# Kernel optimization log

Measured on AMD Instinct MI355X. Metric: run time of the kernel, lower is better.

The kernel has to match this reference:

```python
import jax, jax.numpy as jnp
import numpy as np

N_RAYS = 131072
N_SAMPLES = 128
FEAT_DIM = 3
FAR_DELTA = 1e10  # sentinel delta appended for the last sample, as in the torch code


def setup_inputs() -> dict:
    key = jax.random.key(0)
    k1, k2, k3 = jax.random.split(key, 3)
    # densities are non-negative (output of e.g. relu/softplus in NeRF)
    density = jax.random.uniform(k1, (N_RAYS, N_SAMPLES), dtype=jnp.float32) * 2.0
    feature = jax.random.uniform(k2, (N_RAYS, N_SAMPLES, FEAT_DIM), dtype=jnp.float32)
    # monotonically increasing per-ray sample depths: near + cumsum(uniform bins)
    bins = jax.random.uniform(k3, (N_RAYS, N_SAMPLES), dtype=jnp.float32) * 0.05 + 0.01
    depth_values = 1.0 + jnp.cumsum(bins, axis=1)
    return {"density": density, "feature": feature, "depth_values": depth_values}


def reference(density, feature, depth_values):
    # deltas: consecutive depth differences, with a huge last delta (torch.cat(..., 1e10*ones))
    deltas = jnp.concatenate(
        [depth_values[:, 1:] - depth_values[:, :-1],
         jnp.full_like(depth_values[:, :1], FAR_DELTA)],
        axis=-1,
    )  # [N, S]
    att = jnp.exp(-density * deltas)              # exp(-sigma_i * delta_i), [N, S]
    # inclusive prefix product, matching the loop: T[i] = T[i-1]*exp(-sigma_i*delta_i)
    T = jnp.cumprod(att, axis=1)                  # [N, S]
    weights = T * (1.0 - att)                     # [N, S]
    feat_out = jnp.einsum("ns,nsc->nc", weights, feature)      # [N, 3]
    depth_out = jnp.sum(weights * depth_values, axis=1)         # [N]
    return feat_out, depth_out
```

## Files before the change

### kernel.cpp

```cpp
#include <hip/hip_runtime.h>

#define N_RAYS    131072
#define N_SAMPLES 128
#define FAR_DELTA 1e10f

#define ROW_SHL(n) (0x100 + (n))
#define ROW_SHR(n) (0x110 + (n))
#define QPERM(a,b,c,d) ((a) | ((b) << 2) | ((c) << 4) | ((d) << 6))

template <int CTRL>
__device__ __forceinline__ float dpp_f(float v, float ident) {
    return __int_as_float(__builtin_amdgcn_update_dpp(
        __float_as_int(ident), __float_as_int(v), CTRL, 0xF, 0xF, false));
}

__global__ __launch_bounds__(256) void VolumeRenderer_57612691308835_kernel(
    const float* __restrict__ density,
    const float* __restrict__ feature,
    const float* __restrict__ depth,
    float* __restrict__ out_feat,
    float* __restrict__ out_depth)
{
    const int tid  = threadIdx.x;
    const int wave = tid >> 6;
    const int lane = tid & 63;
    const int p    = lane & 15;
    const int g    = lane >> 4;
    const int ray  = (blockIdx.x << 4) + (wave << 2) + g;

    const long base = (long)ray * N_SAMPLES + p * 8;

    const float4 dn0 = *(const float4*)(density + base);
    const float4 dn1 = *(const float4*)(density + base + 4);
    const float4 dp0 = *(const float4*)(depth + base);
    const float4 dp1 = *(const float4*)(depth + base + 4);
    const float4* fp = (const float4*)(feature + base * 3);
    const float4 f0 = fp[0], f1 = fp[1], f2 = fp[2];
    const float4 f3 = fp[3], f4 = fp[4], f5 = fp[5];

    const float dnext = dpp_f<ROW_SHL(1)>(dp0.x, 0.0f);
    const float d7 = (p == 15) ? FAR_DELTA : (dnext - dp1.w);

    const float a0 = __expf(-dn0.x * (dp0.y - dp0.x));
    const float a1 = __expf(-dn0.y * (dp0.z - dp0.y));
    const float a2 = __expf(-dn0.z * (dp0.w - dp0.z));
    const float a3 = __expf(-dn0.w * (dp1.x - dp0.w));
    const float a4 = __expf(-dn1.x * (dp1.y - dp1.x));
    const float a5 = __expf(-dn1.y * (dp1.z - dp1.y));
    const float a6 = __expf(-dn1.z * (dp1.w - dp1.z));
    const float a7 = __expf(-dn1.w * d7);

    float s = ((a0 * a1) * (a2 * a3)) * ((a4 * a5) * (a6 * a7));
    s *= dpp_f<ROW_SHR(1)>(s, 1.0f);
    s *= dpp_f<ROW_SHR(2)>(s, 1.0f);
    s *= dpp_f<ROW_SHR(4)>(s, 1.0f);
    s *= dpp_f<ROW_SHR(8)>(s, 1.0f);
    float T = dpp_f<ROW_SHR(1)>(s, 1.0f);

    T *= a0; const float w0 = T * (1.0f - a0);
    T *= a1; const float w1 = T * (1.0f - a1);
    T *= a2; const float w2 = T * (1.0f - a2);
    T *= a3; const float w3 = T * (1.0f - a3);
    T *= a4; const float w4 = T * (1.0f - a4);
    T *= a5; const float w5 = T * (1.0f - a5);
    T *= a6; const float w6 = T * (1.0f - a6);
    T *= a7; const float w7 = T * (1.0f - a7);

    float fx = w0*f0.x + w1*f0.w + w2*f1.z + w3*f2.y + w4*f3.x + w5*f3.w + w6*f4.z + w7*f5.y;
    float fy = w0*f0.y + w1*f1.x + w2*f1.w + w3*f2.z + w4*f3.y + w5*f4.x + w6*f4.w + w7*f5.z;
    float fz = w0*f0.z + w1*f1.y + w2*f2.x + w3*f2.w + w4*f3.z + w5*f4.y + w6*f5.x + w7*f5.w;
    float dd = w0*dp0.x + w1*dp0.y + w2*dp0.z + w3*dp0.w + w4*dp1.x + w5*dp1.y + w6*dp1.z + w7*dp1.w;

    fx += dpp_f<ROW_SHL(8)>(fx, 0.0f);
    fy += dpp_f<ROW_SHL(8)>(fy, 0.0f);
    fz += dpp_f<ROW_SHL(8)>(fz, 0.0f);
    dd += dpp_f<ROW_SHL(8)>(dd, 0.0f);
    fx += dpp_f<ROW_SHL(4)>(fx, 0.0f);
    fy += dpp_f<ROW_SHL(4)>(fy, 0.0f);
    fz += dpp_f<ROW_SHL(4)>(fz, 0.0f);
    dd += dpp_f<ROW_SHL(4)>(dd, 0.0f);

    const bool o1 = (p & 1);
    const float sA = o1 ? fx : fy;
    const float rA = dpp_f<QPERM(1, 0, 3, 2)>(sA, 0.0f);
    if (o1) fy += rA; else fx += rA;
    const float sB = o1 ? fz : dd;
    const float rB = dpp_f<QPERM(1, 0, 3, 2)>(sB, 0.0f);
    if (o1) dd += rB; else fz += rB;
    const float own = (p & 2) ? (o1 ? dd : fz) : (o1 ? fy : fx);
    const float sC  = (p & 2) ? (o1 ? fy : fx) : (o1 ? dd : fz);
    const float rC  = dpp_f<QPERM(2, 3, 0, 1)>(sC, 0.0f);
    const float res = own + rC;

    if (p < 3)       out_feat[(long)ray * 3 + p] = res;
    else if (p == 3) out_depth[ray] = res;
}

extern "C" void kernel_launch(void* const* d_in, const int* in_sizes, int n_in,
                              void* d_out, int out_size, void* d_ws, size_t ws_size,
                              hipStream_t stream) {
    const float* density = (const float*)d_in[0];
    const float* feature = (const float*)d_in[1];
    const float* depth   = (const float*)d_in[2];

    float* out_feat  = (float*)d_out;
    float* out_depth = (float*)d_out + (long)N_RAYS * 3;

    const int rays_per_block = 16;
    const int grid = N_RAYS / rays_per_block;
    VolumeRenderer_57612691308835_kernel<<<grid, 256, 0, stream>>>(
        density, feature, depth, out_feat, out_depth);
}
```

Baseline: 352.1 us.

## Persistent waves with register double-buffered coalesced loads staged through LDS

```diff
diff --git a/kernel.cpp b/kernel.cpp
--- a/kernel.cpp
+++ b/kernel.cpp
@@ -3,6 +3,9 @@
 #define N_RAYS    131072
 #define N_SAMPLES 128
 #define FAR_DELTA 1e10f
+
+#define NBLOCKS   1024
+#define ITERS     8
 
 #define ROW_SHL(n) (0x100 + (n))
 #define ROW_SHR(n) (0x110 + (n))
@@ -14,86 +17,162 @@
         __float_as_int(ident), __float_as_int(v), CTRL, 0xF, 0xF, false));
 }
 
-__global__ __launch_bounds__(256) void VolumeRenderer_57612691308835_kernel(
+#define WAVE_LDS  13312
+#define FEAT_STR  112
+#define DD_STR    48
+#define DEN_OFF   7168
+#define DEP_OFF   10240
+
+__global__ __launch_bounds__(256, 3) void VolumeRenderer_57612691308835_kernel(
     const float* __restrict__ density,
     const float* __restrict__ feature,
     const float* __restrict__ depth,
     float* __restrict__ out_feat,
     float* __restrict__ out_depth)
 {
+    __shared__ char lds[4 * WAVE_LDS];
+
     const int tid  = threadIdx.x;
     const int wave = tid >> 6;
     const int lane = tid & 63;
     const int p    = lane & 15;
     const int g    = lane >> 4;
-    const int ray  = (blockIdx.x << 4) + (wave << 2) + g;
 
-    const long base = (long)ray * N_SAMPLES + p * 8;
+    char* wlds = lds + wave * WAVE_LDS;
 
-    const float4 dn0 = *(const float4*)(density + base);
-    const float4 dn1 = *(const float4*)(density + base + 4);
-    const float4 dp0 = *(const float4*)(depth + base);
-    const float4 dp1 = *(const float4*)(depth + base + 4);
-    const float4* fp = (const float4*)(feature + base * 3);
-    const float4 f0 = fp[0], f1 = fp[1], f2 = fp[2];
-    const float4 f3 = fp[3], f4 = fp[4], f5 = fp[5];
+    char* fR  = wlds + lane * FEAT_STR;
+    char* dnR = wlds + DEN_OFF + lane * DD_STR;
+    char* dpR = wlds + DEP_OFF + lane * DD_STR;
 
-    const float dnext = dpp_f<ROW_SHL(1)>(dp0.x, 0.0f);
-    const float d7 = (p == 15) ? FAR_DELTA : (dnext - dp1.w);
+    int wf[6], wdn[2], wdp[2];
+    #pragma unroll
+    for (int c = 0; c < 6; ++c) {
+        const int q  = c * 64 + lane;
+        const int gg = q / 96;
+        const int r  = q - gg * 96;
+        const int pp = r / 6;
+        const int cc = r - pp * 6;
+        wf[c] = gg * (16 * FEAT_STR) + pp * FEAT_STR + cc * 16;
+    }
+    #pragma unroll
+    for (int c = 0; c < 2; ++c) {
+        const int q  = c * 64 + lane;
+        const int gg = q >> 5;
+        const int r  = q & 31;
+        const int pp = r >> 1;
+        const int cc = r & 1;
+        wdn[c] = DEN_OFF + gg * (16 * DD_STR) + pp * DD_STR + cc * 16;
+        wdp[c] = DEP_OFF + gg * (16 * DD_STR) + pp * DD_STR + cc * 16;
+    }
 
-    const float a0 = __expf(-dn0.x * (dp0.y - dp0.x));
-    const float a1 = __expf(-dn0.y * (dp0.z - dp0.y));
-    const float a2 = __expf(-dn0.z * (dp0.w - dp0.z));
-    const float a3 = __expf(-dn0.w * (dp1.x - dp0.w));
-    const float a4 = __expf(-dn1.x * (dp1.y - dp1.x));
-    const float a5 = __expf(-dn1.y * (dp1.z - dp1.y));
-    const float a6 = __expf(-dn1.z * (dp1.w - dp1.z));
-    const float a7 = __expf(-dn1.w * d7);
+    const long wray = ((long)blockIdx.x * 4 + wave) * 32;
+    const float4* fG  = (const float4*)feature + wray * 96 + lane;
+    const float4* dnG = (const float4*)density + wray * 32 + lane;
+    const float4* dpG = (const float4*)depth   + wray * 32 + lane;
 
-    float s = ((a0 * a1) * (a2 * a3)) * ((a4 * a5) * (a6 * a7));
-    s *= dpp_f<ROW_SHR(1)>(s, 1.0f);
-    s *= dpp_f<ROW_SHR(2)>(s, 1.0f);
-    s *= dpp_f<ROW_SHR(4)>(s, 1.0f);
-    s *= dpp_f<ROW_SHR(8)>(s, 1.0f);
-    float T = dpp_f<ROW_SHR(1)>(s, 1.0f);
+    struct Buf { float4 f[6]; float4 dn[2]; float4 dp[2]; };
+    Buf A, B;
 
-    T *= a0; const float w0 = T * (1.0f - a0);
-    T *= a1; const float w1 = T * (1.0f - a1);
-    T *= a2; const float w2 = T * (1.0f - a2);
-    T *= a3; const float w3 = T * (1.0f - a3);
-    T *= a4; const float w4 = T * (1.0f - a4);
-    T *= a5; const float w5 = T * (1.0f - a5);
-    T *= a6; const float w6 = T * (1.0f - a6);
-    T *= a7; const float w7 = T * (1.0f - a7);
+    auto LOAD = [&](Buf& b, int it) {
+        const int fo = it * 384, do_ = it * 128;
+        #pragma unroll
+        for (int c = 0; c < 6; ++c) b.f[c] = fG[fo + c * 64];
+        #pragma unroll
+        for (int c = 0; c < 2; ++c) {
+            b.dn[c] = dnG[do_ + c * 64];
+            b.dp[c] = dpG[do_ + c * 64];
+        }
+    };
 
-    float fx = w0*f0.x + w1*f0.w + w2*f1.z + w3*f2.y + w4*f3.x + w5*f3.w + w6*f4.z + w7*f5.y;
-    float fy = w0*f0.y + w1*f1.x + w2*f1.w + w3*f2.z + w4*f3.y + w5*f4.x + w6*f4.w + w7*f5.z;
-    float fz = w0*f0.z + w1*f1.y + w2*f2.x + w3*f2.w + w4*f3.z + w5*f4.y + w6*f5.x + w7*f5.w;
-    float dd = w0*dp0.x + w1*dp0.y + w2*dp0.z + w3*dp0.w + w4*dp1.x + w5*dp1.y + w6*dp1.z + w7*dp1.w;
+    auto PROC = [&](const Buf& b, int it) {
+        #pragma unroll
+        for (int c = 0; c < 6; ++c) *(float4*)(wlds + wf[c]) = b.f[c];
+        #pragma unroll
+        for (int c = 0; c < 2; ++c) {
+            *(float4*)(wlds + wdn[c]) = b.dn[c];
+            *(float4*)(wlds + wdp[c]) = b.dp[c];
+        }
 
-    fx += dpp_f<ROW_SHL(8)>(fx, 0.0f);
-    fy += dpp_f<ROW_SHL(8)>(fy, 0.0f);
-    fz += dpp_f<ROW_SHL(8)>(fz, 0.0f);
-    dd += dpp_f<ROW_SHL(8)>(dd, 0.0f);
-    fx += dpp_f<ROW_SHL(4)>(fx, 0.0f);
-    fy += dpp_f<ROW_SHL(4)>(fy, 0.0f);
-    fz += dpp_f<ROW_SHL(4)>(fz, 0.0f);
-    dd += dpp_f<ROW_SHL(4)>(dd, 0.0f);
+        const float4 dn0 = *(const float4*)(dnR);
+        const float4 dn1 = *(const float4*)(dnR + 16);
+        const float4 dp0 = *(const float4*)(dpR);
+        const float4 dp1 = *(const float4*)(dpR + 16);
+        const float4 f0 = *(const float4*)(fR);
+        const float4 f1 = *(const float4*)(fR + 16);
+        const float4 f2 = *(const float4*)(fR + 32);
+        const float4 f3 = *(const float4*)(fR + 48);
+        const float4 f4 = *(const float4*)(fR + 64);
+        const float4 f5 = *(const float4*)(fR + 80);
 
-    const bool o1 = (p & 1);
-    const float sA = o1 ? fx : fy;
-    const float rA = dpp_f<QPERM(1, 0, 3, 2)>(sA, 0.0f);
-    if (o1) fy += rA; else fx += rA;
-    const float sB = o1 ? fz : dd;
-    const float rB = dpp_f<QPERM(1, 0, 3, 2)>(sB, 0.0f);
-    if (o1) dd += rB; else fz += rB;
-    const float own = (p & 2) ? (o1 ? dd : fz) : (o1 ? fy : fx);
-    const float sC  = (p & 2) ? (o1 ? fy : fx) : (o1 ? dd : fz);
-    const float rC  = dpp_f<QPERM(2, 3, 0, 1)>(sC, 0.0f);
-    const float res = own + rC;
+        const float dnext = dpp_f<ROW_SHL(1)>(dp0.x, 0.0f);
+        const float d7 = (p == 15) ? FAR_DELTA : (dnext - dp1.w);
 
-    if (p < 3)       out_feat[(long)ray * 3 + p] = res;
-    else if (p == 3) out_depth[ray] = res;
+        const float a0 = __expf(-dn0.x * (dp0.y - dp0.x));
+        const float a1 = __expf(-dn0.y * (dp0.z - dp0.y));
+        const float a2 = __expf(-dn0.z * (dp0.w - dp0.z));
+        const float a3 = __expf(-dn0.w * (dp1.x - dp0.w));
+        const float a4 = __expf(-dn1.x * (dp1.y - dp1.x));
+        const float a5 = __expf(-dn1.y * (dp1.z - dp1.y));
+        const float a6 = __expf(-dn1.z * (dp1.w - dp1.z));
+        const float a7 = __expf(-dn1.w * d7);
+
+        float s = ((a0 * a1) * (a2 * a3)) * ((a4 * a5) * (a6 * a7));
+        s *= dpp_f<ROW_SHR(1)>(s, 1.0f);
+        s *= dpp_f<ROW_SHR(2)>(s, 1.0f);
+        s *= dpp_f<ROW_SHR(4)>(s, 1.0f);
+        s *= dpp_f<ROW_SHR(8)>(s, 1.0f);
+        float T = dpp_f<ROW_SHR(1)>(s, 1.0f);
+
+        T *= a0; const float w0 = T * (1.0f - a0);
+        T *= a1; const float w1 = T * (1.0f - a1);
+        T *= a2; const float w2 = T * (1.0f - a2);
+        T *= a3; const float w3 = T * (1.0f - a3);
+        T *= a4; const float w4 = T * (1.0f - a4);
+        T *= a5; const float w5 = T * (1.0f - a5);
+        T *= a6; const float w6 = T * (1.0f - a6);
+        T *= a7; const float w7 = T * (1.0f - a7);
+
+        float fx = w0*f0.x + w1*f0.w + w2*f1.z + w3*f2.y + w4*f3.x + w5*f3.w + w6*f4.z + w7*f5.y;
+        float fy = w0*f0.y + w1*f1.x + w2*f1.w + w3*f2.z + w4*f3.y + w5*f4.x + w6*f4.w + w7*f5.z;
+        float fz = w0*f0.z + w1*f1.y + w2*f2.x + w3*f2.w + w4*f3.z + w5*f4.y + w6*f5.x + w7*f5.w;
+        float dd = w0*dp0.x + w1*dp0.y + w2*dp0.z + w3*dp0.w + w4*dp1.x + w5*dp1.y + w6*dp1.z + w7*dp1.w;
+
+        fx += dpp_f<ROW_SHL(8)>(fx, 0.0f);
+        fy += dpp_f<ROW_SHL(8)>(fy, 0.0f);
+        fz += dpp_f<ROW_SHL(8)>(fz, 0.0f);
+        dd += dpp_f<ROW_SHL(8)>(dd, 0.0f);
+        fx += dpp_f<ROW_SHL(4)>(fx, 0.0f);
+        fy += dpp_f<ROW_SHL(4)>(fy, 0.0f);
+        fz += dpp_f<ROW_SHL(4)>(fz, 0.0f);
+        dd += dpp_f<ROW_SHL(4)>(dd, 0.0f);
+
+        const bool o1 = (p & 1);
+        const float sA = o1 ? fx : fy;
+        const float rA = dpp_f<QPERM(1, 0, 3, 2)>(sA, 0.0f);
+        float fy2 = fy, fx2 = fx;
+        if (o1) fy2 += rA; else fx2 += rA;
+        const float sB = o1 ? fz : dd;
+        const float rB = dpp_f<QPERM(1, 0, 3, 2)>(sB, 0.0f);
+        float dd2 = dd, fz2 = fz;
+        if (o1) dd2 += rB; else fz2 += rB;
+        const float own = (p & 2) ? (o1 ? dd2 : fz2) : (o1 ? fy2 : fx2);
+        const float sC  = (p & 2) ? (o1 ? fy2 : fx2) : (o1 ? dd2 : fz2);
+        const float rC  = dpp_f<QPERM(2, 3, 0, 1)>(sC, 0.0f);
+        const float res = own + rC;
+
+        const int ray = (int)wray + it * 4 + g;
+        if (p < 3)       out_feat[ray * 3 + p] = res;
+        else if (p == 3) out_depth[ray] = res;
+    };
+
+    LOAD(A, 0);
+    #pragma unroll
+    for (int it = 0; it < ITERS; it += 2) {
+        if (it + 1 < ITERS) LOAD(B, it + 1);
+        PROC(A, it);
+        if (it + 2 < ITERS) LOAD(A, it + 2);
+        PROC(B, it + 1);
+    }
 }
 
 extern "C" void kernel_launch(void* const* d_in, const int* in_sizes, int n_in,
@@ -106,8 +185,6 @@
     float* out_feat  = (float*)d_out;
     float* out_depth = (float*)d_out + (long)N_RAYS * 3;
 
-    const int rays_per_block = 16;
-    const int grid = N_RAYS / rays_per_block;
-    VolumeRenderer_57612691308835_kernel<<<grid, 256, 0, stream>>>(
+    VolumeRenderer_57612691308835_kernel<<<NBLOCKS, 256, 0, stream>>>(
         density, feature, depth, out_feat, out_depth);
 }
```

After: 395.3 us. 12.3% more time.
